# Performance work log

Measured on AMD Instinct MI355X. Metric: run time of the kernel, lower is better.

The kernel has to match this reference:

```python
import jax, jax.numpy as jnp
import numpy as np

B, T, D_IN, H, LAT = 256, 512, 32, 128, 64


def lstm_scan(x, Wih, Whh, bih, bhh):
    """PyTorch-convention single-layer LSTM over x [B,T,D] -> hidden states [B,T,H].
    Gate order: i, f, g, o. Gates = x@Wih.T + bih + h@Whh.T + bhh."""
    Bm, _, _ = x.shape
    Hm = Whh.shape[1]
    # precompute input contributions for all timesteps: [B,T,4H]
    xg = jnp.einsum('btd,gd->btg', x, Wih) + bih + bhh

    def step(carry, g_t):
        h, c = carry
        gates = g_t + h @ Whh.T  # [B,4H]
        i, f, g, o = jnp.split(gates, 4, axis=-1)
        i = jax.nn.sigmoid(i)
        f = jax.nn.sigmoid(f)
        g = jnp.tanh(g)
        o = jax.nn.sigmoid(o)
        c = f * c + i * g
        h = o * jnp.tanh(c)
        return (h, c), h

    h0 = jnp.zeros((Bm, Hm), x.dtype)
    (_, _), hs = jax.lax.scan(step, (h0, h0), jnp.swapaxes(xg, 0, 1))
    return jnp.swapaxes(hs, 0, 1)  # [B,T,H]


def setup_inputs() -> dict:
    key = jax.random.key(0)
    ks = jax.random.split(key, 14)
    s = 1.0 / np.sqrt(H)

    def u(k, shape):
        return jax.random.uniform(k, shape, jnp.float32, -s, s)

    return {
        'x': jax.random.normal(ks[0], (B, T, D_IN), jnp.float32),
        # encoder LSTM (input_dim -> hidden)
        'enc_Wih': u(ks[1], (4 * H, D_IN)),
        'enc_Whh': u(ks[2], (4 * H, H)),
        'enc_bih': u(ks[3], (4 * H,)),
        'enc_bhh': u(ks[4], (4 * H,)),
        # encoder linear (hidden -> latent)
        'enc_Wl': u(ks[5], (LAT, H)),
        'enc_bl': u(ks[6], (LAT,)),
        # decoder LSTM (latent -> hidden)
        'dec_Wih': u(ks[7], (4 * H, LAT)),
        'dec_Whh': u(ks[8], (4 * H, H)),
        'dec_bih': u(ks[9], (4 * H,)),
        'dec_bhh': u(ks[10], (4 * H,)),
        # decoder linear (hidden -> input_dim)
        'dec_Wl': u(ks[11], (D_IN, H)),
        'dec_bl': u(ks[12], (D_IN,)),
    }


def reference(x, enc_Wih, enc_Whh, enc_bih, enc_bhh, enc_Wl, enc_bl,
              dec_Wih, dec_Whh, dec_bih, dec_bhh, dec_Wl, dec_bl):
    # Encoder: last hidden state -> linear -> latent
    hs = lstm_scan(x, enc_Wih, enc_Whh, enc_bih, enc_bhh)  # [B,T,H]
    h_last = hs[:, -1]                                     # == hidden.squeeze(0)
    encoded = h_last @ enc_Wl.T + enc_bl                   # [B,LAT]
    # Decoder: repeat latent over time, LSTM, linear
    z = jnp.broadcast_to(encoded[:, None, :], (encoded.shape[0], T, encoded.shape[1]))
    hs2 = lstm_scan(z, dec_Wih, dec_Whh, dec_bih, dec_bhh)  # [B,T,H]
    decoded = hs2 @ dec_Wl.T + dec_bl                       # [B,T,D_IN]
    return encoded, decoded
```

## Files before the change

kernel.cpp:

```cpp
#include <hip/hip_runtime.h>

#define NB   256
#define NT   512
#define NDIN 32
#define NH   128
#define NLAT 64
#define HSTR 136

typedef _Float16 f16x8 __attribute__((ext_vector_type(8)));
typedef float    f32x4 __attribute__((ext_vector_type(4)));
typedef _Float16 h2    __attribute__((ext_vector_type(2)));
typedef _Float16 h4    __attribute__((ext_vector_type(4)));

__device__ __forceinline__ float dot2(h2 a, h2 b, float c) {
  return __builtin_amdgcn_fdot2(a, b, c, false);
}
__device__ __forceinline__ h2 bc2(float v) { return __builtin_bit_cast(h2, v); }
__device__ __forceinline__ h2 pk2(float a, float b) { return h2{(_Float16)a, (_Float16)b}; }

#define NLOG2E 1.44269504f
__device__ __forceinline__ float sigmoid_f(float x) {
  return __builtin_amdgcn_rcpf(1.f + __builtin_amdgcn_exp2f(x * -NLOG2E));
}
__device__ __forceinline__ float tanh_f(float x) {
  float s = __builtin_amdgcn_rcpf(1.f + __builtin_amdgcn_exp2f(x * (-2.f * NLOG2E)));
  return fmaf(2.f, s, -1.f);
}
__device__ __forceinline__ f32x4 mfma16(f16x8 a, f16x8 b, f32x4 c) {
  return __builtin_amdgcn_mfma_f32_16x16x32_f16(a, b, c, 0, 0, 0);
}

template <int CTRL>
__device__ __forceinline__ float dpp_mov(float v) {
  int p = __builtin_amdgcn_update_dpp(0, __builtin_bit_cast(int, v),
                                      CTRL, 0xF, 0xF, true);
  return __builtin_bit_cast(float, p);
}
#define ROR4  0x124
#define ROR8  0x128
#define ROR12 0x12C

__global__ __launch_bounds__(512, 1) void lstm_ae_kernel(
    const float* __restrict__ x,
    const float* __restrict__ eWih,
    const float* __restrict__ eWhh,
    const float* __restrict__ eBih,
    const float* __restrict__ eBhh,
    const float* __restrict__ eWl,
    const float* __restrict__ eBl,
    const float* __restrict__ dWih,
    const float* __restrict__ dWhh,
    const float* __restrict__ dBih,
    const float* __restrict__ dBhh,
    const float* __restrict__ dWl,
    const float* __restrict__ dBl,
    float* __restrict__ outE,
    float* __restrict__ outD)
{
  extern __shared__ __align__(16) char smem[];
  float*    encs = (float*)smem;
  _Float16* hs   = (_Float16*)(encs + NLAT);
  _Float16* hist = hs + 2 * NH;
  _Float16* xs   = hist;
  float*    gtmp = (float*)(hist + NT * HSTR);

  const int tid = threadIdx.x;
  const int b   = blockIdx.x;
  const int w   = tid >> 6;
  const int l   = tid & 63;
  const int m   = l & 15;
  const int kg  = l >> 4;
  const int ag  = m & 3;
  const int ar  = 2 * (m >> 2);

  int au[4], cu[4];
#pragma unroll
  for (int tt = 0; tt < 4; ++tt) {
    au[tt] = 16 * w + 8 * (tt >> 1) + ar + (tt & 1);
    cu[tt] = 16 * w + 8 * (tt >> 1) + 2 * kg + (tt & 1);
  }
  const bool sb0 = (l & 1) != 0, sb1 = (l & 2) != 0;
  const bool b2  = (l & 4) != 0, b3  = (l & 8) != 0;
  const int  cu_sel = 16 * w + 8 * ((l >> 1) & 1) + 2 * kg + (l & 1);
  const bool writer = (l & 12) == 0;
  const bool gthn   = b3 && !b2;
  const float km = gthn ? (-2.f * NLOG2E) : -NLOG2E;
  const float pa = gthn ? 2.f : 1.f;
  const float pb = gthn ? -1.f : 0.f;

  {
    const float4* xg = (const float4*)(x + (size_t)b * (NT * NDIN));
    h4* xo = (h4*)xs;
#pragma unroll
    for (int i = 0; i < 8; ++i) {
      int idx = i * 512 + tid;
      float4 v = xg[idx];
      xo[idx] = h4{(_Float16)v.x, (_Float16)v.y, (_Float16)v.z, (_Float16)v.w};
    }
  }

  f16x8 aw[4][4];
  f16x8 ax[4];
  f32x4 bi[4];
#pragma unroll
  for (int tt = 0; tt < 4; ++tt) {
    const float* r = eWhh + (size_t)(ag * NH + au[tt]) * NH;
#pragma unroll
    for (int K = 0; K < 4; ++K) {
      const float* p = r + 32 * K + 8 * kg;
#pragma unroll
      for (int j = 0; j < 8; ++j) aw[tt][K][j] = (_Float16)p[j];
    }
    const float* q = eWih + (size_t)(ag * NH + au[tt]) * NDIN + 8 * kg;
#pragma unroll
    for (int j = 0; j < 8; ++j) ax[tt][j] = (_Float16)q[j];
#pragma unroll
    for (int j = 0; j < 4; ++j)
      bi[tt][j] = eBih[j * NH + cu[tt]] + eBhh[j * NH + cu[tt]];
  }
  if (tid < 2 * NH) hs[tid] = (_Float16)0.f;
  float c = 0.f;
  __syncthreads();

  f16x8 xf = *(const f16x8*)(xs + 8 * kg);

#pragma unroll 1
  for (int t = 0; t < NT; ++t) {
    f32x4 acc[4];
    const _Float16* hb = hs + (t & 1) * NH;
    {
#pragma unroll
      for (int tt = 0; tt < 4; ++tt) acc[tt] = mfma16(ax[tt], xf, bi[tt]);
    }
#pragma unroll
    for (int K = 0; K < 4; ++K) {
      f16x8 bf = *(const f16x8*)(hb + 32 * K + 8 * kg);
#pragma unroll
      for (int tt = 0; tt < 4; ++tt) acc[tt] = mfma16(aw[tt][K], bf, acc[tt]);
    }
    float z;
    {
      float v0, v1, v2, v3;
      {
        float u0 = b3 ? acc[0][2] : acc[0][0], u1 = b3 ? acc[0][3] : acc[0][1];
        v0 = b2 ? u1 : u0;
      }
      {
        float u0 = b3 ? acc[1][2] : acc[1][0], u1 = b3 ? acc[1][3] : acc[1][1];
        v1 = b2 ? u1 : u0;
      }
      {
        float u0 = b3 ? acc[2][2] : acc[2][0], u1 = b3 ? acc[2][3] : acc[2][1];
        v2 = b2 ? u1 : u0;
      }
      {
        float u0 = b3 ? acc[3][2] : acc[3][0], u1 = b3 ? acc[3][3] : acc[3][1];
        v3 = b2 ? u1 : u0;
      }
      float w0 = sb1 ? v2 : v0, w1 = sb1 ? v3 : v1;
      z = sb0 ? w1 : w0;
    }
    float a = fmaf(pa, __builtin_amdgcn_rcpf(1.f + __builtin_amdgcn_exp2f(z * km)), pb);
    float vf = dpp_mov<ROR12>(a);
    float vg = dpp_mov<ROR8>(a);
    float vo = dpp_mov<ROR4>(a);
    c = fmaf(vf, c, a * vg);
    float h = vo * tanh_f(c);
    if (writer) hs[((t + 1) & 1) * NH + cu_sel] = (_Float16)h;
    xf = *(const f16x8*)(xs + (((t + 1) & (NT - 1)) * NDIN) + 8 * kg);
    __syncthreads();
  }

  if (tid < NLAT) {
    const float4* p  = (const float4*)(eWl + (size_t)tid * NH);
    const float2* hh = (const float2*)hs;
    float a = eBl[tid];
#pragma unroll
    for (int r = 0; r < 32; ++r) {
      float4 wv = p[r];
      float2 hp = hh[r];
      h2 lov = bc2(hp.x), hiv = bc2(hp.y);
      a = fmaf((float)lov.x, wv.x, a); a = fmaf((float)lov.y, wv.y, a);
      a = fmaf((float)hiv.x, wv.z, a); a = fmaf((float)hiv.y, wv.w, a);
    }
    encs[tid] = a;
    outE[b * NLAT + tid] = a;
  }
#pragma unroll
  for (int tt = 0; tt < 4; ++tt) {
    const float* r = dWhh + (size_t)(ag * NH + au[tt]) * NH;
#pragma unroll
    for (int K = 0; K < 4; ++K) {
      const float* p = r + 32 * K + 8 * kg;
#pragma unroll
      for (int j = 0; j < 8; ++j) aw[tt][K][j] = (_Float16)p[j];
    }
  }
  __syncthreads();

  if (tid < 2 * NH) hs[tid] = (_Float16)0.f;
  {
    const float4* p  = (const float4*)(dWih + (size_t)tid * NLAT);
    const float4* e4 = (const float4*)encs;
    float a = dBih[tid] + dBhh[tid];
#pragma unroll
    for (int r = 0; r < 16; ++r) {
      float4 wv = p[r]; float4 ev = e4[r];
      a = fmaf(ev.x, wv.x, a); a = fmaf(ev.y, wv.y, a);
      a = fmaf(ev.z, wv.z, a); a = fmaf(ev.w, wv.w, a);
    }
    gtmp[tid] = a;
  }
  __syncthreads();
#pragma unroll
  for (int tt = 0; tt < 4; ++tt) {
#pragma unroll
    for (int j = 0; j < 4; ++j) bi[tt][j] = gtmp[j * NH + cu[tt]];
  }
  c = 0.f;

#pragma unroll 1
  for (int t = 0; t < NT; ++t) {
    f32x4 acc[4];
    const _Float16* hb = hs + (t & 1) * NH;
    {
      f16x8 bf = *(const f16x8*)(hb + 8 * kg);
#pragma unroll
      for (int tt = 0; tt < 4; ++tt) acc[tt] = mfma16(aw[tt][0], bf, bi[tt]);
    }
#pragma unroll
    for (int K = 1; K < 4; ++K) {
      f16x8 bf = *(const f16x8*)(hb + 32 * K + 8 * kg);
#pragma unroll
      for (int tt = 0; tt < 4; ++tt) acc[tt] = mfma16(aw[tt][K], bf, acc[tt]);
    }
    float z;
    {
      float v0, v1, v2, v3;
      {
        float u0 = b3 ? acc[0][2] : acc[0][0], u1 = b3 ? acc[0][3] : acc[0][1];
        v0 = b2 ? u1 : u0;
      }
      {
        float u0 = b3 ? acc[1][2] : acc[1][0], u1 = b3 ? acc[1][3] : acc[1][1];
        v1 = b2 ? u1 : u0;
      }
      {
        float u0 = b3 ? acc[2][2] : acc[2][0], u1 = b3 ? acc[2][3] : acc[2][1];
        v2 = b2 ? u1 : u0;
      }
      {
        float u0 = b3 ? acc[3][2] : acc[3][0], u1 = b3 ? acc[3][3] : acc[3][1];
        v3 = b2 ? u1 : u0;
      }
      float w0 = sb1 ? v2 : v0, w1 = sb1 ? v3 : v1;
      z = sb0 ? w1 : w0;
    }
    float a = fmaf(pa, __builtin_amdgcn_rcpf(1.f + __builtin_amdgcn_exp2f(z * km)), pb);
    float vf = dpp_mov<ROR12>(a);
    float vg = dpp_mov<ROR8>(a);
    float vo = dpp_mov<ROR4>(a);
    c = fmaf(vf, c, a * vg);
    float h = vo * tanh_f(c);
    if (writer) {
      _Float16 hh = (_Float16)h;
      hs[((t + 1) & 1) * NH + cu_sel] = hh;
      hist[t * HSTR + cu_sel] = hh;
    }
    __syncthreads();
  }

  {
    const int col = tid & 31, rg = tid >> 5;
    h2 wl[64];
    const float4* p0 = (const float4*)(dWl + (size_t)col * NH);
#pragma unroll
    for (int f = 0; f < 32; ++f) {
      float4 v = p0[f];
      wl[2 * f] = pk2(v.x, v.y); wl[2 * f + 1] = pk2(v.z, v.w);
    }
    const float bo = dBl[col];
    float* op = outD + (size_t)b * (NT * NDIN);
#pragma unroll 1
    for (int i = 0; i < 32; ++i) {
      int r = rg + 16 * i;
      const float4* hp = (const float4*)(hist + r * HSTR);
      float s = 0.f;
#pragma unroll
      for (int j = 0; j < 16; ++j) {
        float4 hvv = hp[j];
        s = dot2(wl[4 * j + 0], bc2(hvv.x), s);
        s = dot2(wl[4 * j + 1], bc2(hvv.y), s);
        s = dot2(wl[4 * j + 2], bc2(hvv.z), s);
        s = dot2(wl[4 * j + 3], bc2(hvv.w), s);
      }
      op[(size_t)r * NDIN + col] = s + bo;
    }
  }
}

#define SMEM_BYTES (NLAT * 4 + 2 * NH * 2 + NT * HSTR * 2 + 512 * 4)

extern "C" void kernel_launch(void* const* d_in, const int* in_sizes, int n_in,
                              void* d_out, int out_size, void* d_ws, size_t ws_size,
                              hipStream_t stream) {
  const float* x    = (const float*)d_in[0];
  const float* eWih = (const float*)d_in[1];
  const float* eWhh = (const float*)d_in[2];
  const float* eBih = (const float*)d_in[3];
  const float* eBhh = (const float*)d_in[4];
  const float* eWl  = (const float*)d_in[5];
  const float* eBl  = (const float*)d_in[6];
  const float* dWih = (const float*)d_in[7];
  const float* dWhh = (const float*)d_in[8];
  const float* dBih = (const float*)d_in[9];
  const float* dBhh = (const float*)d_in[10];
  const float* dWl  = (const float*)d_in[11];
  const float* dBl  = (const float*)d_in[12];

  float* outE = (float*)d_out;
  float* outD = outE + (size_t)NB * NLAT;

  (void)hipFuncSetAttribute((const void*)lstm_ae_kernel,
                            hipFuncAttributeMaxDynamicSharedMemorySize,
                            SMEM_BYTES);

  hipLaunchKernelGGL(lstm_ae_kernel, dim3(NB), dim3(512), SMEM_BYTES, stream,
                     x, eWih, eWhh, eBih, eBhh, eWl, eBl,
                     dWih, dWhh, dBih, dBhh, dWl, dBl, outE, outD);
}
```

Before: 604.7 us.

## Batch 16 samples per block across MFMA columns and split out decoder projection

The main kernel now gives each block 16 samples instead of one, using the MFMA N dimension for the samples, and launches only 16 blocks. Each thread computes all four gates for four hidden units itself rather than spreading them across lanes with DPP rotations. Input x is read from global memory every step. Decoder hidden states go to a workspace buffer, and a second kernel applies the output linear layer. The aim is to stop wasting 15 of 16 MFMA columns, but only 16 CUs are used, and each step now carries many more transcendental ops plus global traffic on the serial critical path.

```diff
diff --git a/kernel.cpp b/kernel.cpp
--- a/kernel.cpp
+++ b/kernel.cpp
@@ -5,7 +5,9 @@
 #define NDIN 32
 #define NH   128
 #define NLAT 64
-#define HSTR 136
+#define SPB  16
+#define NBLK 16
+#define HR   136
 
 typedef _Float16 f16x8 __attribute__((ext_vector_type(8)));
 typedef float    f32x4 __attribute__((ext_vector_type(4)));
@@ -30,17 +32,11 @@
   return __builtin_amdgcn_mfma_f32_16x16x32_f16(a, b, c, 0, 0, 0);
 }
 
-template <int CTRL>
-__device__ __forceinline__ float dpp_mov(float v) {
-  int p = __builtin_amdgcn_update_dpp(0, __builtin_bit_cast(int, v),
-                                      CTRL, 0xF, 0xF, true);
-  return __builtin_bit_cast(float, p);
-}
-#define ROR4  0x124
-#define ROR8  0x128
-#define ROR12 0x12C
-
-__global__ __launch_bounds__(512, 1) void lstm_ae_kernel(
+#define HS_BYTES   (2 * SPB * HR * 2)
+#define ENC_BYTES  (SPB * NLAT * 4)
+#define SMEM_MAIN  (HS_BYTES + ENC_BYTES + SPB * 512 * 4)
+
+__global__ __launch_bounds__(512, 1) void lstm_ae_main(
     const float* __restrict__ x,
     const float* __restrict__ eWih,
     const float* __restrict__ eWhh,
@@ -52,177 +48,158 @@
     const float* __restrict__ dWhh,
     const float* __restrict__ dBih,
     const float* __restrict__ dBhh,
-    const float* __restrict__ dWl,
-    const float* __restrict__ dBl,
-    float* __restrict__ outE,
-    float* __restrict__ outD)
+    _Float16* __restrict__ hist,
+    float* __restrict__ outE)
 {
   extern __shared__ __align__(16) char smem[];
-  float*    encs = (float*)smem;
-  _Float16* hs   = (_Float16*)(encs + NLAT);
-  _Float16* hist = hs + 2 * NH;
-  _Float16* xs   = hist;
-  float*    gtmp = (float*)(hist + NT * HSTR);
+  _Float16* hs   = (_Float16*)smem;
+  float*    encs = (float*)(smem + HS_BYTES);
+  float*    gtmp = (float*)(smem + HS_BYTES + ENC_BYTES);
 
   const int tid = threadIdx.x;
-  const int b   = blockIdx.x;
+  const int bid = blockIdx.x;
   const int w   = tid >> 6;
   const int l   = tid & 63;
-  const int m   = l & 15;
+  const int s   = l & 15;
   const int kg  = l >> 4;
-  const int ag  = m & 3;
-  const int ar  = 2 * (m >> 2);
-
-  int au[4], cu[4];
+  const int ag  = s & 3;
+  const int q   = s >> 2;
+  const int ubase = 16 * w + 4 * kg;
+  const int S   = bid * SPB + s;
+
+  f16x8 aw[4][4];
+  f16x8 axf[4];
+  f32x4 bi[4];
 #pragma unroll
   for (int tt = 0; tt < 4; ++tt) {
-    au[tt] = 16 * w + 8 * (tt >> 1) + ar + (tt & 1);
-    cu[tt] = 16 * w + 8 * (tt >> 1) + 2 * kg + (tt & 1);
-  }
-  const bool sb0 = (l & 1) != 0, sb1 = (l & 2) != 0;
-  const bool b2  = (l & 4) != 0, b3  = (l & 8) != 0;
-  const int  cu_sel = 16 * w + 8 * ((l >> 1) & 1) + 2 * kg + (l & 1);
-  const bool writer = (l & 12) == 0;
-  const bool gthn   = b3 && !b2;
-  const float km = gthn ? (-2.f * NLOG2E) : -NLOG2E;
-  const float pa = gthn ? 2.f : 1.f;
-  const float pb = gthn ? -1.f : 0.f;
-
-  {
-    const float4* xg = (const float4*)(x + (size_t)b * (NT * NDIN));
-    h4* xo = (h4*)xs;
-#pragma unroll
-    for (int i = 0; i < 8; ++i) {
-      int idx = i * 512 + tid;
-      float4 v = xg[idx];
-      xo[idx] = h4{(_Float16)v.x, (_Float16)v.y, (_Float16)v.z, (_Float16)v.w};
-    }
-  }
-
-  f16x8 aw[4][4];
-  f16x8 ax[4];
-  f32x4 bi[4];
+    const int urow = 16 * w + 4 * q + tt;
+    const float* rW = eWhh + (size_t)(ag * NH + urow) * NH;
+#pragma unroll
+    for (int K = 0; K < 4; ++K) {
+      const float* p = rW + 32 * K + 8 * kg;
+#pragma unroll
+      for (int j = 0; j < 8; ++j) aw[tt][K][j] = (_Float16)p[j];
+    }
+    const float* rX = eWih + (size_t)(ag * NH + urow) * NDIN;
+#pragma unroll
+    for (int j = 0; j < 8; ++j) axf[tt][j] = (_Float16)rX[8 * kg + j];
+#pragma unroll
+    for (int j = 0; j < 4; ++j)
+      bi[tt][j] = eBih[j * NH + ubase + tt] + eBhh[j * NH + ubase + tt];
+  }
+  for (int i = tid; i < 2 * SPB * HR; i += 512) hs[i] = (_Float16)0.f;
+  float c0 = 0.f, c1 = 0.f, c2 = 0.f, c3 = 0.f;
+
+  const float* xb = x + (size_t)S * (NT * NDIN) + 8 * kg;
+  float4 cxa = *(const float4*)(xb);
+  float4 cxb = *(const float4*)(xb + 4);
+  __syncthreads();
+
+#pragma unroll 1
+  for (int t = 0; t < NT; ++t) {
+    f16x8 xf;
+    xf[0] = (_Float16)cxa.x; xf[1] = (_Float16)cxa.y;
+    xf[2] = (_Float16)cxa.z; xf[3] = (_Float16)cxa.w;
+    xf[4] = (_Float16)cxb.x; xf[5] = (_Float16)cxb.y;
+    xf[6] = (_Float16)cxb.z; xf[7] = (_Float16)cxb.w;
+    int tn = (t + 1 < NT) ? (t + 1) : (NT - 1);
+    float4 nxa = *(const float4*)(xb + (size_t)tn * NDIN);
+    float4 nxb = *(const float4*)(xb + (size_t)tn * NDIN + 4);
+
+    f32x4 acc[4];
+#pragma unroll
+    for (int tt = 0; tt < 4; ++tt) acc[tt] = mfma16(axf[tt], xf, bi[tt]);
+    const _Float16* hb = hs + (t & 1) * (SPB * HR) + s * HR;
+#pragma unroll
+    for (int K = 0; K < 4; ++K) {
+      f16x8 bf = *(const f16x8*)(hb + 32 * K + 8 * kg);
+#pragma unroll
+      for (int tt = 0; tt < 4; ++tt) acc[tt] = mfma16(aw[tt][K], bf, acc[tt]);
+    }
+    h4 hv;
+    {
+      float gi = sigmoid_f(acc[0][0]), gf = sigmoid_f(acc[0][1]);
+      float gg = tanh_f(acc[0][2]),    go = sigmoid_f(acc[0][3]);
+      c0 = fmaf(gf, c0, gi * gg); hv[0] = (_Float16)(go * tanh_f(c0));
+    }
+    {
+      float gi = sigmoid_f(acc[1][0]), gf = sigmoid_f(acc[1][1]);
+      float gg = tanh_f(acc[1][2]),    go = sigmoid_f(acc[1][3]);
+      c1 = fmaf(gf, c1, gi * gg); hv[1] = (_Float16)(go * tanh_f(c1));
+    }
+    {
+      float gi = sigmoid_f(acc[2][0]), gf = sigmoid_f(acc[2][1]);
+      float gg = tanh_f(acc[2][2]),    go = sigmoid_f(acc[2][3]);
+      c2 = fmaf(gf, c2, gi * gg); hv[2] = (_Float16)(go * tanh_f(c2));
+    }
+    {
+      float gi = sigmoid_f(acc[3][0]), gf = sigmoid_f(acc[3][1]);
+      float gg = tanh_f(acc[3][2]),    go = sigmoid_f(acc[3][3]);
+      c3 = fmaf(gf, c3, gi * gg); hv[3] = (_Float16)(go * tanh_f(c3));
+    }
+    *(h4*)(hs + ((t + 1) & 1) * (SPB * HR) + s * HR + ubase) = hv;
+    cxa = nxa; cxb = nxb;
+    __syncthreads();
+  }
+
+#pragma unroll
+  for (int k = 0; k < 2; ++k) {
+    int idx = tid + 512 * k;
+    int ls = idx >> 6, lat = idx & 63;
+    const float4* p  = (const float4*)(eWl + (size_t)lat * NH);
+    const h2* hh = (const h2*)(hs + ls * HR);
+    float a = eBl[lat];
+#pragma unroll
+    for (int r = 0; r < 32; ++r) {
+      float4 wv = p[r];
+      h2 e0 = hh[2 * r], e1 = hh[2 * r + 1];
+      a = fmaf((float)e0.x, wv.x, a); a = fmaf((float)e0.y, wv.y, a);
+      a = fmaf((float)e1.x, wv.z, a); a = fmaf((float)e1.y, wv.w, a);
+    }
+    encs[ls * NLAT + lat] = a;
+    outE[(size_t)(bid * SPB + ls) * NLAT + lat] = a;
+  }
 #pragma unroll
   for (int tt = 0; tt < 4; ++tt) {
-    const float* r = eWhh + (size_t)(ag * NH + au[tt]) * NH;
+    const int urow = 16 * w + 4 * q + tt;
+    const float* rW = dWhh + (size_t)(ag * NH + urow) * NH;
 #pragma unroll
     for (int K = 0; K < 4; ++K) {
-      const float* p = r + 32 * K + 8 * kg;
+      const float* p = rW + 32 * K + 8 * kg;
 #pragma unroll
       for (int j = 0; j < 8; ++j) aw[tt][K][j] = (_Float16)p[j];
     }
-    const float* q = eWih + (size_t)(ag * NH + au[tt]) * NDIN + 8 * kg;
-#pragma unroll
-    for (int j = 0; j < 8; ++j) ax[tt][j] = (_Float16)q[j];
-#pragma unroll
-    for (int j = 0; j < 4; ++j)
-      bi[tt][j] = eBih[j * NH + cu[tt]] + eBhh[j * NH + cu[tt]];
-  }
-  if (tid < 2 * NH) hs[tid] = (_Float16)0.f;
-  float c = 0.f;
+  }
   __syncthreads();
 
-  f16x8 xf = *(const f16x8*)(xs + 8 * kg);
+  for (int i = tid; i < 2 * SPB * HR; i += 512) hs[i] = (_Float16)0.f;
+#pragma unroll 1
+  for (int k = 0; k < 16; ++k) {
+    int flat = tid + 512 * k;
+    int gs = flat >> 9, ridx = flat & 511;
+    int uu = ridx >> 2, gg2 = ridx & 3;
+    int row = gg2 * NH + uu;
+    const float4* pw = (const float4*)(dWih + (size_t)row * NLAT);
+    const float4* pe = (const float4*)(encs + gs * NLAT);
+    float a = dBih[row] + dBhh[row];
+#pragma unroll
+    for (int r = 0; r < 16; ++r) {
+      float4 wv = pw[r], ev = pe[r];
+      a = fmaf(ev.x, wv.x, a); a = fmaf(ev.y, wv.y, a);
+      a = fmaf(ev.z, wv.z, a); a = fmaf(ev.w, wv.w, a);
+    }
+    gtmp[gs * 512 + ridx] = a;
+  }
+  __syncthreads();
+#pragma unroll
+  for (int tt = 0; tt < 4; ++tt)
+    bi[tt] = *(const f32x4*)(gtmp + s * 512 + 4 * (ubase + tt));
+  c0 = c1 = c2 = c3 = 0.f;
 
 #pragma unroll 1
   for (int t = 0; t < NT; ++t) {
     f32x4 acc[4];
-    const _Float16* hb = hs + (t & 1) * NH;
-    {
-#pragma unroll
-      for (int tt = 0; tt < 4; ++tt) acc[tt] = mfma16(ax[tt], xf, bi[tt]);
-    }
-#pragma unroll
-    for (int K = 0; K < 4; ++K) {
-      f16x8 bf = *(const f16x8*)(hb + 32 * K + 8 * kg);
-#pragma unroll
-      for (int tt = 0; tt < 4; ++tt) acc[tt] = mfma16(aw[tt][K], bf, acc[tt]);
-    }
-    float z;
-    {
-      float v0, v1, v2, v3;
-      {
-        float u0 = b3 ? acc[0][2] : acc[0][0], u1 = b3 ? acc[0][3] : acc[0][1];
-        v0 = b2 ? u1 : u0;
-      }
-      {
-        float u0 = b3 ? acc[1][2] : acc[1][0], u1 = b3 ? acc[1][3] : acc[1][1];
-        v1 = b2 ? u1 : u0;
-      }
-      {
-        float u0 = b3 ? acc[2][2] : acc[2][0], u1 = b3 ? acc[2][3] : acc[2][1];
-        v2 = b2 ? u1 : u0;
-      }
-      {
-        float u0 = b3 ? acc[3][2] : acc[3][0], u1 = b3 ? acc[3][3] : acc[3][1];
-        v3 = b2 ? u1 : u0;
-      }
-      float w0 = sb1 ? v2 : v0, w1 = sb1 ? v3 : v1;
-      z = sb0 ? w1 : w0;
-    }
-    float a = fmaf(pa, __builtin_amdgcn_rcpf(1.f + __builtin_amdgcn_exp2f(z * km)), pb);
-    float vf = dpp_mov<ROR12>(a);
-    float vg = dpp_mov<ROR8>(a);
-    float vo = dpp_mov<ROR4>(a);
-    c = fmaf(vf, c, a * vg);
-    float h = vo * tanh_f(c);
-    if (writer) hs[((t + 1) & 1) * NH + cu_sel] = (_Float16)h;
-    xf = *(const f16x8*)(xs + (((t + 1) & (NT - 1)) * NDIN) + 8 * kg);
-    __syncthreads();
-  }
-
-  if (tid < NLAT) {
-    const float4* p  = (const float4*)(eWl + (size_t)tid * NH);
-    const float2* hh = (const float2*)hs;
-    float a = eBl[tid];
-#pragma unroll
-    for (int r = 0; r < 32; ++r) {
-      float4 wv = p[r];
-      float2 hp = hh[r];
-      h2 lov = bc2(hp.x), hiv = bc2(hp.y);
-      a = fmaf((float)lov.x, wv.x, a); a = fmaf((float)lov.y, wv.y, a);
-      a = fmaf((float)hiv.x, wv.z, a); a = fmaf((float)hiv.y, wv.w, a);
-    }
-    encs[tid] = a;
-    outE[b * NLAT + tid] = a;
-  }
-#pragma unroll
-  for (int tt = 0; tt < 4; ++tt) {
-    const float* r = dWhh + (size_t)(ag * NH + au[tt]) * NH;
-#pragma unroll
-    for (int K = 0; K < 4; ++K) {
-      const float* p = r + 32 * K + 8 * kg;
-#pragma unroll
-      for (int j = 0; j < 8; ++j) aw[tt][K][j] = (_Float16)p[j];
-    }
-  }
-  __syncthreads();
-
-  if (tid < 2 * NH) hs[tid] = (_Float16)0.f;
-  {
-    const float4* p  = (const float4*)(dWih + (size_t)tid * NLAT);
-    const float4* e4 = (const float4*)encs;
-    float a = dBih[tid] + dBhh[tid];
-#pragma unroll
-    for (int r = 0; r < 16; ++r) {
-      float4 wv = p[r]; float4 ev = e4[r];
-      a = fmaf(ev.x, wv.x, a); a = fmaf(ev.y, wv.y, a);
-      a = fmaf(ev.z, wv.z, a); a = fmaf(ev.w, wv.w, a);
-    }
-    gtmp[tid] = a;
-  }
-  __syncthreads();
-#pragma unroll
-  for (int tt = 0; tt < 4; ++tt) {
-#pragma unroll
-    for (int j = 0; j < 4; ++j) bi[tt][j] = gtmp[j * NH + cu[tt]];
-  }
-  c = 0.f;
-
-#pragma unroll 1
-  for (int t = 0; t < NT; ++t) {
-    f32x4 acc[4];
-    const _Float16* hb = hs + (t & 1) * NH;
+    const _Float16* hb = hs + (t & 1) * (SPB * HR) + s * HR;
     {
       f16x8 bf = *(const f16x8*)(hb + 8 * kg);
 #pragma unroll
@@ -234,72 +211,67 @@
 #pragma unroll
       for (int tt = 0; tt < 4; ++tt) acc[tt] = mfma16(aw[tt][K], bf, acc[tt]);
     }
-    float z;
-    {
-      float v0, v1, v2, v3;
-      {
-        float u0 = b3 ? acc[0][2] : acc[0][0], u1 = b3 ? acc[0][3] : acc[0][1];
-        v0 = b2 ? u1 : u0;
-      }
-      {
-        float u0 = b3 ? acc[1][2] : acc[1][0], u1 = b3 ? acc[1][3] : acc[1][1];
-        v1 = b2 ? u1 : u0;
-      }
-      {
-        float u0 = b3 ? acc[2][2] : acc[2][0], u1 = b3 ? acc[2][3] : acc[2][1];
-        v2 = b2 ? u1 : u0;
-      }
-      {
-        float u0 = b3 ? acc[3][2] : acc[3][0], u1 = b3 ? acc[3][3] : acc[3][1];
-        v3 = b2 ? u1 : u0;
-      }
-      float w0 = sb1 ? v2 : v0, w1 = sb1 ? v3 : v1;
-      z = sb0 ? w1 : w0;
-    }
-    float a = fmaf(pa, __builtin_amdgcn_rcpf(1.f + __builtin_amdgcn_exp2f(z * km)), pb);
-    float vf = dpp_mov<ROR12>(a);
-    float vg = dpp_mov<ROR8>(a);
-    float vo = dpp_mov<ROR4>(a);
-    c = fmaf(vf, c, a * vg);
-    float h = vo * tanh_f(c);
-    if (writer) {
-      _Float16 hh = (_Float16)h;
-      hs[((t + 1) & 1) * NH + cu_sel] = hh;
-      hist[t * HSTR + cu_sel] = hh;
-    }
+    h4 hv;
+    {
+      float gi = sigmoid_f(acc[0][0]), gf = sigmoid_f(acc[0][1]);
+      float gg = tanh_f(acc[0][2]),    go = sigmoid_f(acc[0][3]);
+      c0 = fmaf(gf, c0, gi * gg); hv[0] = (_Float16)(go * tanh_f(c0));
+    }
+    {
+      float gi = sigmoid_f(acc[1][0]), gf = sigmoid_f(acc[1][1]);
+      float gg = tanh_f(acc[1][2]),    go = sigmoid_f(acc[1][3]);
+      c1 = fmaf(gf, c1, gi * gg); hv[1] = (_Float16)(go * tanh_f(c1));
+    }
+    {
+      float gi = sigmoid_f(acc[2][0]), gf = sigmoid_f(acc[2][1]);
+      float gg = tanh_f(acc[2][2]),    go = sigmoid_f(acc[2][3]);
+      c2 = fmaf(gf, c2, gi * gg); hv[2] = (_Float16)(go * tanh_f(c2));
+    }
+    {
+      float gi = sigmoid_f(acc[3][0]), gf = sigmoid_f(acc[3][1]);
+      float gg = tanh_f(acc[3][2]),    go = sigmoid_f(acc[3][3]);
+      c3 = fmaf(gf, c3, gi * gg); hv[3] = (_Float16)(go * tanh_f(c3));
+    }
+    *(h4*)(hs + ((t + 1) & 1) * (SPB * HR) + s * HR + ubase) = hv;
+    *(h4*)(hist + ((size_t)S * NT + t) * NH + ubase) = hv;
     __syncthreads();
   }
-
-  {
-    const int col = tid & 31, rg = tid >> 5;
-    h2 wl[64];
-    const float4* p0 = (const float4*)(dWl + (size_t)col * NH);
-#pragma unroll
-    for (int f = 0; f < 32; ++f) {
-      float4 v = p0[f];
-      wl[2 * f] = pk2(v.x, v.y); wl[2 * f + 1] = pk2(v.z, v.w);
-    }
-    const float bo = dBl[col];
-    float* op = outD + (size_t)b * (NT * NDIN);
+}
+
+__global__ __launch_bounds__(512, 1) void lstm_ae_epi(
+    const _Float16* __restrict__ hist,
+    const float* __restrict__ dWl,
+    const float* __restrict__ dBl,
+    float* __restrict__ outD)
+{
+  const int tid = threadIdx.x;
+  const int b   = blockIdx.x;
+  const int col = tid & 31, rg = tid >> 5;
+  h2 wl[64];
+  const float4* p0 = (const float4*)(dWl + (size_t)col * NH);
+#pragma unroll
+  for (int f = 0; f < 32; ++f) {
+    float4 v = p0[f];
+    wl[2 * f] = pk2(v.x, v.y); wl[2 * f + 1] = pk2(v.z, v.w);
+  }
+  const float bo = dBl[col];
+  float* op = outD + (size_t)b * (NT * NDIN);
 #pragma unroll 1
-    for (int i = 0; i < 32; ++i) {
-      int r = rg + 16 * i;
-      const float4* hp = (const float4*)(hist + r * HSTR);
-      float s = 0.f;
-#pragma unroll
-      for (int j = 0; j < 16; ++j) {
-        float4 hvv = hp[j];
-        s = dot2(wl[4 * j + 0], bc2(hvv.x), s);
-        s = dot2(wl[4 * j + 1], bc2(hvv.y), s);
-        s = dot2(wl[4 * j + 2], bc2(hvv.z), s);
-        s = dot2(wl[4 * j + 3], bc2(hvv.w), s);
-      }
-      op[(size_t)r * NDIN + col] = s + bo;
-    }
-  }
-}
-
-#define SMEM_BYTES (NLAT * 4 + 2 * NH * 2 + NT * HSTR * 2 + 512 * 4)
+  for (int i = 0; i < 32; ++i) {
+    int r = rg + 16 * i;
+    const float4* hp = (const float4*)(hist + ((size_t)b * NT + r) * NH);
+    float sacc = 0.f;
+#pragma unroll
+    for (int j = 0; j < 16; ++j) {
+      float4 hvv = hp[j];
+      sacc = dot2(wl[4 * j + 0], bc2(hvv.x), sacc);
+      sacc = dot2(wl[4 * j + 1], bc2(hvv.y), sacc);
+      sacc = dot2(wl[4 * j + 2], bc2(hvv.z), sacc);
+      sacc = dot2(wl[4 * j + 3], bc2(hvv.w), sacc);
+    }
+    op[(size_t)r * NDIN + col] = sacc + bo;
+  }
+}
 
 extern "C" void kernel_launch(void* const* d_in, const int* in_sizes, int n_in,
                               void* d_out, int out_size, void* d_ws, size_t ws_size,
@@ -320,12 +292,15 @@
 
   float* outE = (float*)d_out;
   float* outD = outE + (size_t)NB * NLAT;
-
-  (void)hipFuncSetAttribute((const void*)lstm_ae_kernel,
+  _Float16* hist = (_Float16*)d_ws;
+
+  (void)hipFuncSetAttribute((const void*)lstm_ae_main,
                             hipFuncAttributeMaxDynamicSharedMemorySize,
-                            SMEM_BYTES);
-
-  hipLaunchKernelGGL(lstm_ae_kernel, dim3(NB), dim3(512), SMEM_BYTES, stream,
+                            SMEM_MAIN);
+
+  hipLaunchKernelGGL(lstm_ae_main, dim3(NBLK), dim3(512), SMEM_MAIN, stream,
                      x, eWih, eWhh, eBih, eBhh, eWl, eBl,
-                     dWih, dWhh, dBih, dBhh, dWl, dBl, outE, outD);
-}
+                     dWih, dWhh, dBih, dBhh, hist, outE);
+  hipLaunchKernelGGL(lstm_ae_epi, dim3(NB), dim3(512), 0, stream,
+                     hist, dWl, dBl, outD);
+}
```

New measurement: 957.3 us. 58.3% more time.
